# Kernel optimization log

Measured on AMD Instinct MI355X. Metric: run time of the kernel, lower is better.

The kernel has to match this reference:

```python
import jax, jax.numpy as jnp
import numpy as np

EPS = 1e-5
NUM_HEADS = 4


def setup_inputs() -> dict:
    key = jax.random.key(0)
    ks = jax.random.split(key, 10)
    B, C, H, W = 16, 512, 32, 32
    s = 1.0 / np.sqrt(C)
    x = jax.random.normal(ks[0], (B, C, H, W), dtype=jnp.float32)
    gn_weight = jnp.ones((C,), jnp.float32)
    gn_bias = jnp.zeros((C,), jnp.float32)
    wq = jax.random.uniform(ks[1], (C, C), jnp.float32, -s, s)
    bq = jax.random.uniform(ks[2], (C,), jnp.float32, -s, s)
    wk = jax.random.uniform(ks[3], (C, C), jnp.float32, -s, s)
    bk = jax.random.uniform(ks[4], (C,), jnp.float32, -s, s)
    wv = jax.random.uniform(ks[5], (C, C), jnp.float32, -s, s)
    bv = jax.random.uniform(ks[6], (C,), jnp.float32, -s, s)
    wo = jax.random.uniform(ks[7], (C, C), jnp.float32, -s, s)
    bo = jax.random.uniform(ks[8], (C,), jnp.float32, -s, s)
    return dict(x=x, gn_weight=gn_weight, gn_bias=gn_bias, wq=wq, bq=bq,
                wk=wk, bk=bk, wv=wv, bv=bv, wo=wo, bo=bo)


def reference(x, gn_weight, gn_bias, wq, bq, wk, bk, wv, bv, wo, bo):
    B, C, H, W = x.shape
    head_size = C // NUM_HEADS

    # GroupNorm(num_groups=1): normalize over (C,H,W) per batch element
    mean = jnp.mean(x, axis=(1, 2, 3), keepdims=True)
    var = jnp.var(x, axis=(1, 2, 3), keepdims=True)
    xn = (x - mean) / jnp.sqrt(var + EPS)
    xn = xn * gn_weight[None, :, None, None] + gn_bias[None, :, None, None]

    # (B, C, H, W) -> (B, S, C) with S = H*W
    seq = xn.reshape(B, C, H * W).transpose(0, 2, 1)

    def heads(y):  # (B, S, C) -> (B, nh, S, hd)
        return y.reshape(B, H * W, NUM_HEADS, head_size).transpose(0, 2, 1, 3)

    q = heads(seq @ wq.T + bq)
    k = heads(seq @ wk.T + bk)
    v = heads(seq @ wv.T + bv)

    scores = jnp.einsum('bhqd,bhkd->bhqk', q, k) / np.sqrt(head_size).astype(np.float32)
    attn = jax.nn.softmax(scores, axis=-1)
    out = jnp.einsum('bhqk,bhkd->bhqd', attn, v)  # (B, nh, S, hd)

    out = out.transpose(0, 2, 1, 3).reshape(B, H * W, C)
    out = out @ wo.T + bo
    out = out.transpose(0, 2, 1).reshape(B, C, H, W)
    return out + x
```

## Files before the change

### kernel.cpp

```cpp
#include <hip/hip_runtime.h>
#include <stdint.h>

#define B_  16
#define C_  512
#define S_  1024
#define NH  4
#define HD  128
#define BS  (B_*S_)

typedef __attribute__((ext_vector_type(8))) short   short8;
typedef __attribute__((ext_vector_type(4))) float   f32x4;
typedef __attribute__((ext_vector_type(4))) unsigned int uint4v;

__device__ __forceinline__ unsigned short f2bf(float f) {
    unsigned u = __float_as_uint(f);
    unsigned r = (u + 0x7fffu + ((u >> 16) & 1u)) >> 16;
    return (unsigned short)r;
}

__device__ __forceinline__ unsigned cvt_pk_bf16(float a, float b) {
    unsigned r;
    asm("v_cvt_pk_bf16_f32 %0, %1, %2" : "=v"(r) : "v"(a), "v"(b));
    return r;
}

__global__ void gn_partial(const float* __restrict__ x, float* __restrict__ part) {
    int b = blockIdx.x, chunk = blockIdx.y;
    const float4* xb = (const float4*)(x + (size_t)b * C_ * S_);
    int base = chunk * 4096 + threadIdx.x;
    float s = 0.f, ss = 0.f;
#pragma unroll
    for (int i = 0; i < 16; ++i) {
        float4 v = xb[base + i * 256];
        s  += v.x + v.y + v.z + v.w;
        ss += v.x*v.x + v.y*v.y + v.z*v.z + v.w*v.w;
    }
    for (int off = 32; off; off >>= 1) { s += __shfl_down(s, off); ss += __shfl_down(ss, off); }
    __shared__ float red[2][4];
    int wv = threadIdx.x >> 6;
    if ((threadIdx.x & 63) == 0) { red[0][wv] = s; red[1][wv] = ss; }
    __syncthreads();
    if (threadIdx.x == 0) {
        s  = red[0][0] + red[0][1] + red[0][2] + red[0][3];
        ss = red[1][0] + red[1][1] + red[1][2] + red[1][3];
        part[(b*32 + chunk)*2 + 0] = s;
        part[(b*32 + chunk)*2 + 1] = ss;
    }
}

__global__ void gn_apply_t(const float* __restrict__ x, const float* __restrict__ part,
                           const float* __restrict__ gw, const float* __restrict__ gb,
                           unsigned short* __restrict__ seq) {
    int st = blockIdx.x, ct = blockIdx.y, b = blockIdx.z;
    float s1 = 0.f, s2 = 0.f;
#pragma unroll
    for (int i = 0; i < 32; ++i) { s1 += part[(b*32+i)*2]; s2 += part[(b*32+i)*2+1]; }
    const float invN = 1.0f / (float)(C_ * S_);
    float mean = s1 * invN;
    float var  = s2 * invN - mean * mean;
    float rstd = rsqrtf(var + 1e-5f);

    __shared__ unsigned short tile[64][72];
    int c0 = ct * 64, s0 = st * 64;
    const float* xb = x + ((size_t)b * C_ + c0) * S_ + s0;
    int tr = threadIdx.x >> 4, tj = (threadIdx.x & 15) * 4;
#pragma unroll
    for (int p = 0; p < 4; ++p) {
        int i = tr + p * 16;
        float w  = gw[c0 + i];
        float bb = gb[c0 + i];
        float4 v = *(const float4*)(xb + (size_t)i * S_ + tj);
        tile[i][tj+0] = f2bf((v.x - mean) * rstd * w + bb);
        tile[i][tj+1] = f2bf((v.y - mean) * rstd * w + bb);
        tile[i][tj+2] = f2bf((v.z - mean) * rstd * w + bb);
        tile[i][tj+3] = f2bf((v.w - mean) * rstd * w + bb);
    }
    __syncthreads();
    int j  = threadIdx.x >> 2;
    int cc = (threadIdx.x & 3) * 16;
    unsigned short tmp[16] __attribute__((aligned(16)));
#pragma unroll
    for (int i = 0; i < 16; ++i) tmp[i] = tile[cc + i][j];
    unsigned short* dst = seq + ((size_t)(b * S_ + s0 + j)) * C_ + c0 + cc;
    *(uint4v*)dst       = *(uint4v*)tmp;
    *(uint4v*)(dst + 8) = *(uint4v*)(tmp + 8);
}

__global__ void cvt_w(const float* __restrict__ wq, const float* __restrict__ wk,
                      const float* __restrict__ wv, const float* __restrict__ wo,
                      unsigned short* __restrict__ wqkv, unsigned short* __restrict__ wobf) {
    int m = blockIdx.y;
    const float* src = (m == 0) ? wq : (m == 1) ? wk : (m == 2) ? wv : wo;
    unsigned short* dst = (m < 3) ? (wqkv + (size_t)m * C_ * C_) : wobf;
    int i = blockIdx.x * 256 + threadIdx.x;
    float4 v = ((const float4*)src)[i];
    unsigned short o[4] __attribute__((aligned(8)));
    o[0] = f2bf(v.x); o[1] = f2bf(v.y); o[2] = f2bf(v.z); o[3] = f2bf(v.w);
    *(unsigned long long*)(dst + (size_t)i * 4) = *(unsigned long long*)o;
}

__device__ __forceinline__ void gemm128_bt(const unsigned short* __restrict__ Ab,
                                           const unsigned short* __restrict__ Bb,
                                           const int K,
                                           unsigned short* lA, unsigned short* lB,
                                           f32x4 acc[4][4]) {
    const int t = threadIdx.x;
    const int w = t >> 6, l = t & 63;
    const int wr = (w >> 1) * 64, wc = (w & 1) * 64;
    const int lrow = l & 15;
    const int lk8  = (l >> 4) * 8;
#pragma unroll
    for (int mi = 0; mi < 4; ++mi)
#pragma unroll
        for (int ni = 0; ni < 4; ++ni)
            acc[mi][ni] = (f32x4){0.f, 0.f, 0.f, 0.f};

    for (int kt = 0; kt < K; kt += 64) {
#pragma unroll
        for (int j = 0; j < 4; ++j) {
            const int lin = j * 256 + t;
            const int row = lin >> 3, ch = lin & 7;
            __builtin_amdgcn_global_load_lds(
                (const __attribute__((address_space(1))) unsigned int*)(Ab + (size_t)row * K + kt + ch * 8),
                (__attribute__((address_space(3))) unsigned int*)(lA + (size_t)(j * 256 + w * 64) * 8),
                16, 0, 0);
        }
#pragma unroll
        for (int j = 0; j < 4; ++j) {
            const int lin = j * 256 + t;
            const int row = lin >> 3, ch = lin & 7;
            __builtin_amdgcn_global_load_lds(
                (const __attribute__((address_space(1))) unsigned int*)(Bb + (size_t)row * K + kt + ch * 8),
                (__attribute__((address_space(3))) unsigned int*)(lB + (size_t)(j * 256 + w * 64) * 8),
                16, 0, 0);
        }
        __syncthreads();
#pragma unroll
        for (int kk = 0; kk < 2; ++kk) {
            short8 af[4], bf[4];
            const int ko = lk8 + kk * 32;
#pragma unroll
            for (int mi = 0; mi < 4; ++mi)
                af[mi] = *(const short8*)&lA[(size_t)(wr + mi * 16 + lrow) * 64 + ko];
#pragma unroll
            for (int ni = 0; ni < 4; ++ni)
                bf[ni] = *(const short8*)&lB[(size_t)(wc + ni * 16 + lrow) * 64 + ko];
#pragma unroll
            for (int mi = 0; mi < 4; ++mi)
#pragma unroll
                for (int ni = 0; ni < 4; ++ni)
                    acc[mi][ni] = __builtin_amdgcn_mfma_f32_16x16x32_bf16(af[mi], bf[ni], acc[mi][ni], 0, 0, 0);
        }
        __syncthreads();
    }
}

__global__ __launch_bounds__(256) void qkv_gemm(
        const unsigned short* __restrict__ seq, const unsigned short* __restrict__ wqkv,
        const float* __restrict__ bq, const float* __restrict__ bk, const float* __restrict__ bv,
        unsigned short* __restrict__ qb, unsigned short* __restrict__ kb, unsigned short* __restrict__ vb) {
    __shared__ unsigned short lA[128 * 64], lB[128 * 64];
    int mb = blockIdx.x, nb = blockIdx.y;
    f32x4 acc[4][4];
    gemm128_bt(seq + (size_t)mb * 128 * C_, wqkv + (size_t)nb * 128 * C_, C_, lA, lB, acc);

    int mat = nb >> 2;
    const float* bias = (mat == 0) ? bq : (mat == 1) ? bk : bv;
    unsigned short* out = (mat == 0) ? qb : (mat == 1) ? kb : vb;
    float oscale = (mat == 0) ? 0.12751879523087253f : 1.0f;
    int cb = (nb & 3) * 128;

    int w = threadIdx.x >> 6, l = threadIdx.x & 63;
    int wr = (w >> 1) * 64, wc = (w & 1) * 64;
#pragma unroll
    for (int mi = 0; mi < 4; ++mi)
#pragma unroll
        for (int ni = 0; ni < 4; ++ni)
#pragma unroll
            for (int r = 0; r < 4; ++r) {
                int m = mb * 128 + wr + mi * 16 + (l >> 4) * 4 + r;
                int c = cb + wc + ni * 16 + (l & 15);
                int b = m >> 10, s = m & 1023;
                int h = c >> 7,  d = c & 127;
                float v = (acc[mi][ni][r] + bias[c]) * oscale;
                out[(((size_t)(b * NH + h) * S_) + s) * HD + d] = f2bf(v);
            }
}

__global__ void v_transpose(const unsigned short* __restrict__ v, unsigned short* __restrict__ vt) {
    int st = blockIdx.x, dt = blockIdx.y, bh = blockIdx.z;
    __shared__ unsigned short tile[64][72];
    const unsigned short* src = v + ((size_t)bh * S_ + st * 64) * HD + dt * 64;
    int ti = threadIdx.x >> 3, tj = (threadIdx.x & 7) * 8;
#pragma unroll
    for (int p = 0; p < 2; ++p) {
        int i = ti + p * 32;
        *(uint4v*)&tile[i][tj] = *(const uint4v*)(src + (size_t)i * HD + tj);
    }
    __syncthreads();
    unsigned short* dst = vt + ((size_t)bh * HD + dt * 64) * S_ + st * 64;
    int j = threadIdx.x >> 2, sc = (threadIdx.x & 3) * 16;
    unsigned short tmp[16] __attribute__((aligned(16)));
#pragma unroll
    for (int i = 0; i < 16; ++i) tmp[i] = tile[sc + i][j];
    unsigned short* dp = dst + (size_t)j * S_ + sc;
    *(uint4v*)dp       = *(uint4v*)tmp;
    *(uint4v*)(dp + 8) = *(uint4v*)(tmp + 8);
}

__global__ __launch_bounds__(256) void flash_attn(
        const unsigned short* __restrict__ q, const unsigned short* __restrict__ k,
        const unsigned short* __restrict__ vt, unsigned short* __restrict__ o) {
    int bh = blockIdx.x, qblk = blockIdx.y;
    int t = threadIdx.x, w = t >> 6, l = t & 63;
    int l15 = l & 15, g = l >> 4;
    int swz = (l15 & 7) << 1;
    __shared__ unsigned short lK[64 * 128];
    __shared__ unsigned short lV[128 * 64];
    __shared__ unsigned short lP[4][16 * 64];

    const size_t bh_base = (size_t)bh * S_ * HD;
    int q0 = qblk * 64;

    short8 qf[4];
    const unsigned short* qp = q + bh_base + (size_t)(q0 + w * 16 + l15) * HD + g * 8;
#pragma unroll
    for (int dc = 0; dc < 4; ++dc) qf[dc] = *(const short8*)(qp + dc * 32);

    f32x4 oacc[8];
#pragma unroll
    for (int i = 0; i < 8; ++i) oacc[i] = (f32x4){0.f, 0.f, 0.f, 0.f};
    float m_run = -1e30f, l_run = 0.f;
    unsigned short* myP = &lP[w][0];

    for (int kt = 0; kt < 16; ++kt) {
        int kv0 = kt * 64;
#pragma unroll
        for (int j = 0; j < 4; ++j) {
            int lin = j * 256 + t;
            int row = lin >> 4, c16 = lin & 15;
            int sc  = (c16 & 8) | ((c16 ^ row) & 7);
            __builtin_amdgcn_global_load_lds(
                (const __attribute__((address_space(1))) unsigned int*)(k + bh_base + (size_t)(kv0 + row) * HD + sc * 8),
                (__attribute__((address_space(3))) unsigned int*)(lK + (size_t)(j * 256 + w * 64) * 8),
                16, 0, 0);
        }
#pragma unroll
        for (int j = 0; j < 4; ++j) {
            int lin = j * 256 + t;
            int row = lin >> 3, c16 = lin & 7;
            int sc  = (c16 ^ row) & 7;
            __builtin_amdgcn_global_load_lds(
                (const __attribute__((address_space(1))) unsigned int*)(vt + bh_base + (size_t)row * S_ + kv0 + sc * 8),
                (__attribute__((address_space(3))) unsigned int*)(lV + (size_t)(j * 256 + w * 64) * 8),
                16, 0, 0);
        }
        __syncthreads();

        f32x4 sfr[4];
#pragma unroll
        for (int nb = 0; nb < 4; ++nb) {
            sfr[nb] = (f32x4){0.f, 0.f, 0.f, 0.f};
#pragma unroll
            for (int kc = 0; kc < 4; ++kc) {
                int row = nb * 16 + l15;
                int gg  = g + kc * 4;
                int ch  = (gg & 8) | ((gg ^ row) & 7);
                short8 kf = *(const short8*)&lK[(size_t)row * 128 + ch * 8];
                sfr[nb] = __builtin_amdgcn_mfma_f32_16x16x32_bf16(kf, qf[kc], sfr[nb], 0, 0, 0);
            }
        }

        float mx = sfr[0][0];
        mx = fmaxf(mx, sfr[0][1]); mx = fmaxf(mx, sfr[0][2]); mx = fmaxf(mx, sfr[0][3]);
#pragma unroll
        for (int nb = 1; nb < 4; ++nb) {
            mx = fmaxf(mx, fmaxf(fmaxf(sfr[nb][0], sfr[nb][1]), fmaxf(sfr[nb][2], sfr[nb][3])));
        }
        mx = fmaxf(mx, __shfl_xor(mx, 16));
        mx = fmaxf(mx, __shfl_xor(mx, 32));

        if (!__all(mx - m_run <= 8.f)) {
            float mnew  = fmaxf(m_run, mx);
            float alpha = exp2f(m_run - mnew);
            m_run = mnew;
            l_run *= alpha;
            float ar0 = __shfl(alpha, g * 4 + 0);
            float ar1 = __shfl(alpha, g * 4 + 1);
            float ar2 = __shfl(alpha, g * 4 + 2);
            float ar3 = __shfl(alpha, g * 4 + 3);
#pragma unroll
            for (int dn = 0; dn < 8; ++dn) {
                oacc[dn][0] *= ar0; oacc[dn][1] *= ar1;
                oacc[dn][2] *= ar2; oacc[dn][3] *= ar3;
            }
        }

        float psum = 0.f;
#pragma unroll
        for (int nb = 0; nb < 4; ++nb) {
            float p0 = exp2f(sfr[nb][0] - m_run);
            float p1 = exp2f(sfr[nb][1] - m_run);
            float p2 = exp2f(sfr[nb][2] - m_run);
            float p3 = exp2f(sfr[nb][3] - m_run);
            psum += (p0 + p1) + (p2 + p3);
            unsigned d0 = cvt_pk_bf16(p0, p1);
            unsigned d1 = cvt_pk_bf16(p2, p3);
            int c = (nb * 4 + g) ^ swz;
            *(unsigned long long*)(myP + l15 * 64 + c * 4) =
                (unsigned long long)d0 | ((unsigned long long)d1 << 32);
        }
        psum += __shfl_xor(psum, 16);
        psum += __shfl_xor(psum, 32);
        l_run += psum;

#pragma unroll
        for (int kc = 0; kc < 2; ++kc) {
            int c0 = (kc * 8 + g * 2)     ^ swz;
            int c1 = (kc * 8 + g * 2 + 1) ^ swz;
            union { unsigned long long u[2]; short8 v; } pf;
            pf.u[0] = *(const unsigned long long*)(myP + l15 * 64 + c0 * 4);
            pf.u[1] = *(const unsigned long long*)(myP + l15 * 64 + c1 * 4);
            int pg = g + kc * 4;
#pragma unroll
            for (int dn = 0; dn < 8; ++dn) {
                int vrow = dn * 16 + l15;
                int vch  = (pg ^ vrow) & 7;
                short8 vf = *(const short8*)&lV[(size_t)vrow * 64 + vch * 8];
                oacc[dn] = __builtin_amdgcn_mfma_f32_16x16x32_bf16(pf.v, vf, oacc[dn], 0, 0, 0);
            }
        }
        __syncthreads();
    }

    float linv = 1.0f / l_run;
    float i0 = __shfl(linv, g * 4 + 0);
    float i1 = __shfl(linv, g * 4 + 1);
    float i2 = __shfl(linv, g * 4 + 2);
    float i3 = __shfl(linv, g * 4 + 3);
    int b = bh >> 2, h = bh & 3;
    int srow = q0 + w * 16 + g * 4;
#pragma unroll
    for (int dn = 0; dn < 8; ++dn) {
        int cbase = h * HD + dn * 16 + l15;
        o[((size_t)(b * S_ + srow + 0)) * C_ + cbase] = f2bf(oacc[dn][0] * i0);
        o[((size_t)(b * S_ + srow + 1)) * C_ + cbase] = f2bf(oacc[dn][1] * i1);
        o[((size_t)(b * S_ + srow + 2)) * C_ + cbase] = f2bf(oacc[dn][2] * i2);
        o[((size_t)(b * S_ + srow + 3)) * C_ + cbase] = f2bf(oacc[dn][3] * i3);
    }
}

__global__ __launch_bounds__(256) void oproj_gemm(
        const unsigned short* __restrict__ wobf, const unsigned short* __restrict__ attn,
        const float* __restrict__ bo, const float* __restrict__ x, float* __restrict__ out) {
    int cbk = blockIdx.x, sb = blockIdx.y, b = blockIdx.z;
    __shared__ unsigned short lA[128 * 64], lB[128 * 64];
    f32x4 acc[4][4];
    gemm128_bt(wobf + (size_t)cbk * 128 * C_,
               attn + ((size_t)b * S_ + sb * 128) * C_, C_, lA, lB, acc);

    int w = threadIdx.x >> 6, l = threadIdx.x & 63;
    int wr = (w >> 1) * 64, wc = (w & 1) * 64;
#pragma unroll
    for (int mi = 0; mi < 4; ++mi)
#pragma unroll
        for (int ni = 0; ni < 4; ++ni)
#pragma unroll
            for (int r = 0; r < 4; ++r) {
                int c = cbk * 128 + wr + mi * 16 + (l >> 4) * 4 + r;
                int s = sb * 128 + wc + ni * 16 + (l & 15);
                size_t off = ((size_t)b * C_ + c) * S_ + s;
                out[off] = acc[mi][ni][r] + bo[c] + x[off];
            }
}

extern "C" void kernel_launch(void* const* d_in, const int* in_sizes, int n_in,
                              void* d_out, int out_size, void* d_ws, size_t ws_size,
                              hipStream_t stream) {
    const float* x  = (const float*)d_in[0];
    const float* gw = (const float*)d_in[1];
    const float* gb = (const float*)d_in[2];
    const float* wq = (const float*)d_in[3];
    const float* bq = (const float*)d_in[4];
    const float* wk = (const float*)d_in[5];
    const float* bk = (const float*)d_in[6];
    const float* wv = (const float*)d_in[7];
    const float* bv = (const float*)d_in[8];
    const float* wo = (const float*)d_in[9];
    const float* bo = (const float*)d_in[10];
    float* out = (float*)d_out;

    char* ws = (char*)d_ws;
    const size_t SEQ_BYTES = (size_t)BS * C_ * 2;
    float* part           = (float*)ws;
    unsigned short* seq   = (unsigned short*)(ws + 4096);
    unsigned short* wqkv  = (unsigned short*)(ws + 4096 + SEQ_BYTES);
    unsigned short* wobf  = (unsigned short*)(ws + 4096 + SEQ_BYTES + 1572864);
    unsigned short* qb    = (unsigned short*)(ws + 4096 + SEQ_BYTES + 1572864 + 524288);
    unsigned short* kb    = qb + 8388608;
    unsigned short* vb    = kb + 8388608;
    unsigned short* vtb   = vb + 8388608;
    unsigned short* attn  = seq;

    gn_partial<<<dim3(16, 32), 256, 0, stream>>>(x, part);
    gn_apply_t<<<dim3(16, 8, 16), 256, 0, stream>>>(x, part, gw, gb, seq);
    cvt_w<<<dim3(256, 4), 256, 0, stream>>>(wq, wk, wv, wo, wqkv, wobf);
    qkv_gemm<<<dim3(128, 12), 256, 0, stream>>>(seq, wqkv, bq, bk, bv, qb, kb, vb);
    v_transpose<<<dim3(16, 2, 64), 256, 0, stream>>>(vb, vtb);
    flash_attn<<<dim3(64, 16), 256, 0, stream>>>(qb, kb, vtb, attn);
    oproj_gemm<<<dim3(4, 8, 16), 256, 0, stream>>>(wobf, attn, bo, x, out);
}
```

Measured before the change: 165.4 us.

## Fuse V transpose into QKV GEMM epilogue and double-buffer flash attention with 32 queries per wave

The V-projection epilogue now writes a transposed tile through shared memory straight into the V^T buffer, so the separate v_transpose kernel and its extra global round trip go away. Flash attention now double-buffers its K/V tiles, prefetching the next tile while the current one is computed. Each wave also processes 32 query rows instead of 16, so every K/V fragment read from LDS is reused twice and half as many blocks are launched. The cost is higher register and LDS use per block, which can lower occupancy, and a grid of 512 blocks may fill the CUs less evenly.

```diff
diff --git a/kernel.cpp b/kernel.cpp
--- a/kernel.cpp
+++ b/kernel.cpp
@@ -158,54 +158,62 @@
 __global__ __launch_bounds__(256) void qkv_gemm(
         const unsigned short* __restrict__ seq, const unsigned short* __restrict__ wqkv,
         const float* __restrict__ bq, const float* __restrict__ bk, const float* __restrict__ bv,
-        unsigned short* __restrict__ qb, unsigned short* __restrict__ kb, unsigned short* __restrict__ vb) {
-    __shared__ unsigned short lA[128 * 64], lB[128 * 64];
+        unsigned short* __restrict__ qb, unsigned short* __restrict__ kb, unsigned short* __restrict__ vtb) {
+    __shared__ unsigned short sbuf[128 * 136];
+    unsigned short* lA = sbuf;
+    unsigned short* lB = sbuf + 128 * 64;
     int mb = blockIdx.x, nb = blockIdx.y;
     f32x4 acc[4][4];
     gemm128_bt(seq + (size_t)mb * 128 * C_, wqkv + (size_t)nb * 128 * C_, C_, lA, lB, acc);
 
     int mat = nb >> 2;
-    const float* bias = (mat == 0) ? bq : (mat == 1) ? bk : bv;
-    unsigned short* out = (mat == 0) ? qb : (mat == 1) ? kb : vb;
-    float oscale = (mat == 0) ? 0.12751879523087253f : 1.0f;
     int cb = (nb & 3) * 128;
-
     int w = threadIdx.x >> 6, l = threadIdx.x & 63;
+    int l15 = l & 15, g = l >> 4;
     int wr = (w >> 1) * 64, wc = (w & 1) * 64;
-#pragma unroll
-    for (int mi = 0; mi < 4; ++mi)
-#pragma unroll
-        for (int ni = 0; ni < 4; ++ni)
-#pragma unroll
-            for (int r = 0; r < 4; ++r) {
-                int m = mb * 128 + wr + mi * 16 + (l >> 4) * 4 + r;
-                int c = cb + wc + ni * 16 + (l & 15);
-                int b = m >> 10, s = m & 1023;
-                int h = c >> 7,  d = c & 127;
-                float v = (acc[mi][ni][r] + bias[c]) * oscale;
-                out[(((size_t)(b * NH + h) * S_) + s) * HD + d] = f2bf(v);
+
+    if (mat < 2) {
+        const float* bias = (mat == 0) ? bq : bk;
+        unsigned short* out = (mat == 0) ? qb : kb;
+        float oscale = (mat == 0) ? 0.12751879523087253f : 1.0f;
+#pragma unroll
+        for (int mi = 0; mi < 4; ++mi)
+#pragma unroll
+            for (int ni = 0; ni < 4; ++ni)
+#pragma unroll
+                for (int r = 0; r < 4; ++r) {
+                    int m = mb * 128 + wr + mi * 16 + g * 4 + r;
+                    int c = cb + wc + ni * 16 + l15;
+                    int b = m >> 10, s = m & 1023;
+                    int h = c >> 7,  d = c & 127;
+                    float v = (acc[mi][ni][r] + bias[c]) * oscale;
+                    out[(((size_t)(b * NH + h) * S_) + s) * HD + d] = f2bf(v);
+                }
+    } else {
+        int b  = mb >> 3;
+        int s0 = (mb & 7) * 128;
+        int h  = nb & 3;
+#pragma unroll
+        for (int mi = 0; mi < 4; ++mi)
+#pragma unroll
+            for (int ni = 0; ni < 4; ++ni) {
+                int dloc = wc + ni * 16 + l15;
+                int mloc = wr + mi * 16 + g * 4;
+                float bia = bv[h * 128 + dloc];
+#pragma unroll
+                for (int r = 0; r < 4; ++r)
+                    sbuf[dloc * 136 + mloc + r] = f2bf(acc[mi][ni][r] + bia);
             }
-}
-
-__global__ void v_transpose(const unsigned short* __restrict__ v, unsigned short* __restrict__ vt) {
-    int st = blockIdx.x, dt = blockIdx.y, bh = blockIdx.z;
-    __shared__ unsigned short tile[64][72];
-    const unsigned short* src = v + ((size_t)bh * S_ + st * 64) * HD + dt * 64;
-    int ti = threadIdx.x >> 3, tj = (threadIdx.x & 7) * 8;
-#pragma unroll
-    for (int p = 0; p < 2; ++p) {
-        int i = ti + p * 32;
-        *(uint4v*)&tile[i][tj] = *(const uint4v*)(src + (size_t)i * HD + tj);
-    }
-    __syncthreads();
-    unsigned short* dst = vt + ((size_t)bh * HD + dt * 64) * S_ + st * 64;
-    int j = threadIdx.x >> 2, sc = (threadIdx.x & 3) * 16;
-    unsigned short tmp[16] __attribute__((aligned(16)));
-#pragma unroll
-    for (int i = 0; i < 16; ++i) tmp[i] = tile[sc + i][j];
-    unsigned short* dp = dst + (size_t)j * S_ + sc;
-    *(uint4v*)dp       = *(uint4v*)tmp;
-    *(uint4v*)(dp + 8) = *(uint4v*)(tmp + 8);
+        __syncthreads();
+        unsigned short* dst = vtb + ((size_t)(b * NH + h)) * HD * S_ + s0;
+#pragma unroll
+        for (int p = 0; p < 8; ++p) {
+            int idx = p * 256 + threadIdx.x;
+            int d = idx >> 4, cc = (idx & 15) * 8;
+            short8 vv = *(const short8*)&sbuf[d * 136 + cc];
+            *(short8*)(dst + (size_t)d * S_ + cc) = vv;
+        }
+    }
 }
 
 __global__ __launch_bounds__(256) void flash_attn(
@@ -215,138 +223,162 @@
     int t = threadIdx.x, w = t >> 6, l = t & 63;
     int l15 = l & 15, g = l >> 4;
     int swz = (l15 & 7) << 1;
-    __shared__ unsigned short lK[64 * 128];
-    __shared__ unsigned short lV[128 * 64];
-    __shared__ unsigned short lP[4][16 * 64];
+    __shared__ unsigned short lK[2][64 * 128];
+    __shared__ unsigned short lV[2][128 * 64];
+    __shared__ unsigned short lP[4][32 * 64];
 
     const size_t bh_base = (size_t)bh * S_ * HD;
-    int q0 = qblk * 64;
-
-    short8 qf[4];
-    const unsigned short* qp = q + bh_base + (size_t)(q0 + w * 16 + l15) * HD + g * 8;
-#pragma unroll
-    for (int dc = 0; dc < 4; ++dc) qf[dc] = *(const short8*)(qp + dc * 32);
-
-    f32x4 oacc[8];
-#pragma unroll
-    for (int i = 0; i < 8; ++i) oacc[i] = (f32x4){0.f, 0.f, 0.f, 0.f};
-    float m_run = -1e30f, l_run = 0.f;
+    int q0 = qblk * 128 + w * 32;
+
+    short8 qa[4], qb_[4];
+    const unsigned short* qp = q + bh_base + (size_t)(q0 + l15) * HD + g * 8;
+#pragma unroll
+    for (int kc = 0; kc < 4; ++kc) {
+        qa[kc]  = *(const short8*)(qp + kc * 32);
+        qb_[kc] = *(const short8*)(qp + 16 * HD + kc * 32);
+    }
+
+    f32x4 oa[8], ob[8];
+#pragma unroll
+    for (int i = 0; i < 8; ++i) { oa[i] = (f32x4){0.f,0.f,0.f,0.f}; ob[i] = (f32x4){0.f,0.f,0.f,0.f}; }
+    float m_a = -1e30f, l_a = 0.f, m_b = -1e30f, l_b = 0.f;
     unsigned short* myP = &lP[w][0];
 
+#define STAGE_TILE(buf, kv0_) do {                                                     \
+    int kv0s = (kv0_);                                                                 \
+    _Pragma("unroll")                                                                  \
+    for (int j = 0; j < 4; ++j) {                                                      \
+        int lin = j * 256 + t;                                                         \
+        int row = lin >> 4, c16 = lin & 15;                                            \
+        int sc  = (c16 & 8) | ((c16 ^ row) & 7);                                       \
+        __builtin_amdgcn_global_load_lds(                                              \
+            (const __attribute__((address_space(1))) unsigned int*)(k + bh_base + (size_t)(kv0s + row) * HD + sc * 8), \
+            (__attribute__((address_space(3))) unsigned int*)(&lK[buf][0] + (size_t)(j * 256 + w * 64) * 8), \
+            16, 0, 0);                                                                 \
+    }                                                                                  \
+    _Pragma("unroll")                                                                  \
+    for (int j = 0; j < 4; ++j) {                                                      \
+        int lin = j * 256 + t;                                                         \
+        int row = lin >> 3, c8 = lin & 7;                                              \
+        int sc  = (c8 ^ row) & 7;                                                      \
+        __builtin_amdgcn_global_load_lds(                                              \
+            (const __attribute__((address_space(1))) unsigned int*)(vt + bh_base + (size_t)row * S_ + kv0s + sc * 8), \
+            (__attribute__((address_space(3))) unsigned int*)(&lV[buf][0] + (size_t)(j * 256 + w * 64) * 8), \
+            16, 0, 0);                                                                 \
+    }                                                                                  \
+} while (0)
+
+    STAGE_TILE(0, 0);
+    __syncthreads();
+    int cur = 0;
+
     for (int kt = 0; kt < 16; ++kt) {
-        int kv0 = kt * 64;
-#pragma unroll
-        for (int j = 0; j < 4; ++j) {
-            int lin = j * 256 + t;
-            int row = lin >> 4, c16 = lin & 15;
-            int sc  = (c16 & 8) | ((c16 ^ row) & 7);
-            __builtin_amdgcn_global_load_lds(
-                (const __attribute__((address_space(1))) unsigned int*)(k + bh_base + (size_t)(kv0 + row) * HD + sc * 8),
-                (__attribute__((address_space(3))) unsigned int*)(lK + (size_t)(j * 256 + w * 64) * 8),
-                16, 0, 0);
-        }
-#pragma unroll
-        for (int j = 0; j < 4; ++j) {
-            int lin = j * 256 + t;
-            int row = lin >> 3, c16 = lin & 7;
-            int sc  = (c16 ^ row) & 7;
-            __builtin_amdgcn_global_load_lds(
-                (const __attribute__((address_space(1))) unsigned int*)(vt + bh_base + (size_t)row * S_ + kv0 + sc * 8),
-                (__attribute__((address_space(3))) unsigned int*)(lV + (size_t)(j * 256 + w * 64) * 8),
-                16, 0, 0);
-        }
-        __syncthreads();
-
-        f32x4 sfr[4];
+        if (kt < 15) STAGE_TILE(cur ^ 1, (kt + 1) * 64);
+        const unsigned short* lKc = &lK[cur][0];
+        const unsigned short* lVc = &lV[cur][0];
+
+        f32x4 sa[4], sb[4];
 #pragma unroll
         for (int nb = 0; nb < 4; ++nb) {
-            sfr[nb] = (f32x4){0.f, 0.f, 0.f, 0.f};
-#pragma unroll
-            for (int kc = 0; kc < 4; ++kc) {
+            sa[nb] = (f32x4){0.f,0.f,0.f,0.f};
+            sb[nb] = (f32x4){0.f,0.f,0.f,0.f};
+        }
+#pragma unroll
+        for (int kc = 0; kc < 4; ++kc)
+#pragma unroll
+            for (int nb = 0; nb < 4; ++nb) {
                 int row = nb * 16 + l15;
                 int gg  = g + kc * 4;
                 int ch  = (gg & 8) | ((gg ^ row) & 7);
-                short8 kf = *(const short8*)&lK[(size_t)row * 128 + ch * 8];
-                sfr[nb] = __builtin_amdgcn_mfma_f32_16x16x32_bf16(kf, qf[kc], sfr[nb], 0, 0, 0);
+                short8 kf = *(const short8*)&lKc[(size_t)row * 128 + ch * 8];
+                sa[nb] = __builtin_amdgcn_mfma_f32_16x16x32_bf16(kf, qa[kc],  sa[nb], 0, 0, 0);
+                sb[nb] = __builtin_amdgcn_mfma_f32_16x16x32_bf16(kf, qb_[kc], sb[nb], 0, 0, 0);
             }
-        }
-
-        float mx = sfr[0][0];
-        mx = fmaxf(mx, sfr[0][1]); mx = fmaxf(mx, sfr[0][2]); mx = fmaxf(mx, sfr[0][3]);
+
+        float mxa = fmaxf(fmaxf(sa[0][0], sa[0][1]), fmaxf(sa[0][2], sa[0][3]));
+        float mxb = fmaxf(fmaxf(sb[0][0], sb[0][1]), fmaxf(sb[0][2], sb[0][3]));
 #pragma unroll
         for (int nb = 1; nb < 4; ++nb) {
-            mx = fmaxf(mx, fmaxf(fmaxf(sfr[nb][0], sfr[nb][1]), fmaxf(sfr[nb][2], sfr[nb][3])));
-        }
-        mx = fmaxf(mx, __shfl_xor(mx, 16));
-        mx = fmaxf(mx, __shfl_xor(mx, 32));
-
-        if (!__all(mx - m_run <= 8.f)) {
-            float mnew  = fmaxf(m_run, mx);
-            float alpha = exp2f(m_run - mnew);
-            m_run = mnew;
-            l_run *= alpha;
-            float ar0 = __shfl(alpha, g * 4 + 0);
-            float ar1 = __shfl(alpha, g * 4 + 1);
-            float ar2 = __shfl(alpha, g * 4 + 2);
-            float ar3 = __shfl(alpha, g * 4 + 3);
+            mxa = fmaxf(mxa, fmaxf(fmaxf(sa[nb][0], sa[nb][1]), fmaxf(sa[nb][2], sa[nb][3])));
+            mxb = fmaxf(mxb, fmaxf(fmaxf(sb[nb][0], sb[nb][1]), fmaxf(sb[nb][2], sb[nb][3])));
+        }
+        mxa = fmaxf(mxa, __shfl_xor(mxa, 16)); mxa = fmaxf(mxa, __shfl_xor(mxa, 32));
+        mxb = fmaxf(mxb, __shfl_xor(mxb, 16)); mxb = fmaxf(mxb, __shfl_xor(mxb, 32));
+
+        if (!__all((mxa - m_a <= 8.f) && (mxb - m_b <= 8.f))) {
+            float mna = fmaxf(m_a, mxa), mnb = fmaxf(m_b, mxb);
+            float ala = exp2f(m_a - mna), alb = exp2f(m_b - mnb);
+            m_a = mna; m_b = mnb; l_a *= ala; l_b *= alb;
+            float a0 = __shfl(ala, g*4+0), a1 = __shfl(ala, g*4+1),
+                  a2 = __shfl(ala, g*4+2), a3 = __shfl(ala, g*4+3);
+            float b0 = __shfl(alb, g*4+0), b1 = __shfl(alb, g*4+1),
+                  b2 = __shfl(alb, g*4+2), b3 = __shfl(alb, g*4+3);
 #pragma unroll
             for (int dn = 0; dn < 8; ++dn) {
-                oacc[dn][0] *= ar0; oacc[dn][1] *= ar1;
-                oacc[dn][2] *= ar2; oacc[dn][3] *= ar3;
+                oa[dn][0] *= a0; oa[dn][1] *= a1; oa[dn][2] *= a2; oa[dn][3] *= a3;
+                ob[dn][0] *= b0; ob[dn][1] *= b1; ob[dn][2] *= b2; ob[dn][3] *= b3;
             }
         }
 
-        float psum = 0.f;
+        float psa = 0.f, psb = 0.f;
 #pragma unroll
         for (int nb = 0; nb < 4; ++nb) {
-            float p0 = exp2f(sfr[nb][0] - m_run);
-            float p1 = exp2f(sfr[nb][1] - m_run);
-            float p2 = exp2f(sfr[nb][2] - m_run);
-            float p3 = exp2f(sfr[nb][3] - m_run);
-            psum += (p0 + p1) + (p2 + p3);
-            unsigned d0 = cvt_pk_bf16(p0, p1);
-            unsigned d1 = cvt_pk_bf16(p2, p3);
+            float p0 = exp2f(sa[nb][0] - m_a), p1 = exp2f(sa[nb][1] - m_a);
+            float p2 = exp2f(sa[nb][2] - m_a), p3 = exp2f(sa[nb][3] - m_a);
+            psa += (p0 + p1) + (p2 + p3);
+            unsigned d0 = cvt_pk_bf16(p0, p1), d1 = cvt_pk_bf16(p2, p3);
             int c = (nb * 4 + g) ^ swz;
             *(unsigned long long*)(myP + l15 * 64 + c * 4) =
                 (unsigned long long)d0 | ((unsigned long long)d1 << 32);
-        }
-        psum += __shfl_xor(psum, 16);
-        psum += __shfl_xor(psum, 32);
-        l_run += psum;
+            float r0 = exp2f(sb[nb][0] - m_b), r1 = exp2f(sb[nb][1] - m_b);
+            float r2 = exp2f(sb[nb][2] - m_b), r3 = exp2f(sb[nb][3] - m_b);
+            psb += (r0 + r1) + (r2 + r3);
+            unsigned e0 = cvt_pk_bf16(r0, r1), e1 = cvt_pk_bf16(r2, r3);
+            *(unsigned long long*)(myP + (l15 + 16) * 64 + c * 4) =
+                (unsigned long long)e0 | ((unsigned long long)e1 << 32);
+        }
+        psa += __shfl_xor(psa, 16); psa += __shfl_xor(psa, 32);
+        psb += __shfl_xor(psb, 16); psb += __shfl_xor(psb, 32);
+        l_a += psa; l_b += psb;
 
 #pragma unroll
         for (int kc = 0; kc < 2; ++kc) {
-            int c0 = (kc * 8 + g * 2)     ^ swz;
-            int c1 = (kc * 8 + g * 2 + 1) ^ swz;
-            union { unsigned long long u[2]; short8 v; } pf;
-            pf.u[0] = *(const unsigned long long*)(myP + l15 * 64 + c0 * 4);
-            pf.u[1] = *(const unsigned long long*)(myP + l15 * 64 + c1 * 4);
+            int c0 = (kc * 8 + g * 2) ^ swz;
+            short8 pa = *(const short8*)(myP + l15 * 64 + c0 * 4);
+            short8 pb = *(const short8*)(myP + (l15 + 16) * 64 + c0 * 4);
             int pg = g + kc * 4;
 #pragma unroll
             for (int dn = 0; dn < 8; ++dn) {
                 int vrow = dn * 16 + l15;
                 int vch  = (pg ^ vrow) & 7;
-                short8 vf = *(const short8*)&lV[(size_t)vrow * 64 + vch * 8];
-                oacc[dn] = __builtin_amdgcn_mfma_f32_16x16x32_bf16(pf.v, vf, oacc[dn], 0, 0, 0);
+                short8 vf = *(const short8*)&lVc[(size_t)vrow * 64 + vch * 8];
+                oa[dn] = __builtin_amdgcn_mfma_f32_16x16x32_bf16(pa, vf, oa[dn], 0, 0, 0);
+                ob[dn] = __builtin_amdgcn_mfma_f32_16x16x32_bf16(pb, vf, ob[dn], 0, 0, 0);
             }
         }
         __syncthreads();
-    }
-
-    float linv = 1.0f / l_run;
-    float i0 = __shfl(linv, g * 4 + 0);
-    float i1 = __shfl(linv, g * 4 + 1);
-    float i2 = __shfl(linv, g * 4 + 2);
-    float i3 = __shfl(linv, g * 4 + 3);
+        cur ^= 1;
+    }
+#undef STAGE_TILE
+
+    float ia = 1.0f / l_a, ib = 1.0f / l_b;
+    float ia0 = __shfl(ia, g*4+0), ia1 = __shfl(ia, g*4+1),
+          ia2 = __shfl(ia, g*4+2), ia3 = __shfl(ia, g*4+3);
+    float ib0 = __shfl(ib, g*4+0), ib1 = __shfl(ib, g*4+1),
+          ib2 = __shfl(ib, g*4+2), ib3 = __shfl(ib, g*4+3);
     int b = bh >> 2, h = bh & 3;
-    int srow = q0 + w * 16 + g * 4;
+    int sra = q0 + g * 4;
 #pragma unroll
     for (int dn = 0; dn < 8; ++dn) {
         int cbase = h * HD + dn * 16 + l15;
-        o[((size_t)(b * S_ + srow + 0)) * C_ + cbase] = f2bf(oacc[dn][0] * i0);
-        o[((size_t)(b * S_ + srow + 1)) * C_ + cbase] = f2bf(oacc[dn][1] * i1);
-        o[((size_t)(b * S_ + srow + 2)) * C_ + cbase] = f2bf(oacc[dn][2] * i2);
-        o[((size_t)(b * S_ + srow + 3)) * C_ + cbase] = f2bf(oacc[dn][3] * i3);
+        o[((size_t)(b * S_ + sra + 0)) * C_ + cbase]  = f2bf(oa[dn][0] * ia0);
+        o[((size_t)(b * S_ + sra + 1)) * C_ + cbase]  = f2bf(oa[dn][1] * ia1);
+        o[((size_t)(b * S_ + sra + 2)) * C_ + cbase]  = f2bf(oa[dn][2] * ia2);
+        o[((size_t)(b * S_ + sra + 3)) * C_ + cbase]  = f2bf(oa[dn][3] * ia3);
+        o[((size_t)(b * S_ + sra + 16)) * C_ + cbase] = f2bf(ob[dn][0] * ib0);
+        o[((size_t)(b * S_ + sra + 17)) * C_ + cbase] = f2bf(ob[dn][1] * ib1);
+        o[((size_t)(b * S_ + sra + 18)) * C_ + cbase] = f2bf(ob[dn][2] * ib2);
+        o[((size_t)(b * S_ + sra + 19)) * C_ + cbase] = f2bf(ob[dn][3] * ib3);
     }
 }
 
@@ -398,15 +430,13 @@
     unsigned short* wobf  = (unsigned short*)(ws + 4096 + SEQ_BYTES + 1572864);
     unsigned short* qb    = (unsigned short*)(ws + 4096 + SEQ_BYTES + 1572864 + 524288);
     unsigned short* kb    = qb + 8388608;
-    unsigned short* vb    = kb + 8388608;
-    unsigned short* vtb   = vb + 8388608;
+    unsigned short* vtb   = kb + 8388608;
     unsigned short* attn  = seq;
 
     gn_partial<<<dim3(16, 32), 256, 0, stream>>>(x, part);
     gn_apply_t<<<dim3(16, 8, 16), 256, 0, stream>>>(x, part, gw, gb, seq);
     cvt_w<<<dim3(256, 4), 256, 0, stream>>>(wq, wk, wv, wo, wqkv, wobf);
-    qkv_gemm<<<dim3(128, 12), 256, 0, stream>>>(seq, wqkv, bq, bk, bv, qb, kb, vb);
-    v_transpose<<<dim3(16, 2, 64), 256, 0, stream>>>(vb, vtb);
-    flash_attn<<<dim3(64, 16), 256, 0, stream>>>(qb, kb, vtb, attn);
+    qkv_gemm<<<dim3(128, 12), 256, 0, stream>>>(seq, wqkv, bq, bk, bv, qb, kb, vtb);
+    flash_attn<<<dim3(64, 8), 256, 0, stream>>>(qb, kb, vtb, attn);
     oproj_gemm<<<dim3(4, 8, 16), 256, 0, stream>>>(wobf, attn, bo, x, out);
 }
```

Measured after the change: 147.2 us, median of 2. -11.0%, faster.
